# Performance work log

Hardware: AMD Instinct MI355X
Metric: run time of the kernel (lower is better)

The kernel has to match this reference:

```python
import jax, jax.numpy as jnp
import numpy as np

B, T, E = 4, 2048, 1024
H, D = 16, 64  # num_heads, head_size; H*D == E


def setup_inputs() -> dict:
    key = jax.random.key(0)
    ks = jax.random.split(key, 8)
    s = 0.02
    x = jax.random.normal(ks[0], (B, T, E), dtype=jnp.float32)
    attention_mask = jnp.ones((B, T), dtype=jnp.float32)
    # stacked per-head projection weights (no bias), torch Linear: y = x @ W.T
    Wq = jax.random.normal(ks[1], (H, E, D), dtype=jnp.float32) * s
    Wk = jax.random.normal(ks[2], (H, E, D), dtype=jnp.float32) * s
    Wv = jax.random.normal(ks[3], (H, E, D), dtype=jnp.float32) * s
    Wo = jax.random.normal(ks[4], (E, E), dtype=jnp.float32) * s
    bo = jnp.zeros((E,), dtype=jnp.float32)
    return {"x": x, "attention_mask": attention_mask, "Wq": Wq, "Wk": Wk,
            "Wv": Wv, "Wo": Wo, "bo": bo}


def reference(x, attention_mask, Wq, Wk, Wv, Wo, bo):
    # per-head projections, vectorized over heads: [B,T,E] x [H,E,D] -> [B,H,T,D]
    q = jnp.einsum('bte,hed->bhtd', x, Wq)
    k = jnp.einsum('bte,hed->bhtd', x, Wk)
    v = jnp.einsum('bte,hed->bhtd', x, Wv)
    scores = jnp.einsum('bhtd,bhsd->bhts', q, k) / jnp.sqrt(jnp.float32(D))
    # causal mask (tril): masked_fill with -inf
    causal = jnp.tril(jnp.ones((T, T), dtype=bool))
    scores = jnp.where(causal[None, None, :, :], scores, -jnp.inf)
    # padding mask: weights += (1 - mask) * finfo(float32).min, broadcast over queries
    neg = jnp.finfo(jnp.float32).min
    scores = scores + ((1.0 - attention_mask) * neg)[:, None, None, :]
    weights = jax.nn.softmax(scores, axis=-1)
    out = jnp.einsum('bhts,bhsd->bthd', weights, v).reshape(B, T, H * D)
    return out @ Wo.T + bo
```

## Files before the change

### kernel.cpp

```cpp
#include <hip/hip_runtime.h>
#include <hip/hip_bf16.h>

#define B_ 4
#define T_ 2048
#define E_ 1024
#define H_ 16
#define D_ 64
#define M_ (B_*T_)

typedef short bf16x8 __attribute__((ext_vector_type(8)));
typedef float f32x4  __attribute__((ext_vector_type(4)));
typedef float f32x16 __attribute__((ext_vector_type(16)));

__device__ __forceinline__ short f2bf(float f) {
    __hip_bfloat16 h = __float2bfloat16(f);
    return *reinterpret_cast<short*>(&h);
}

__device__ __forceinline__ void async_ld16(const void* g, void* l) {
    __builtin_amdgcn_global_load_lds(
        (const __attribute__((address_space(1))) unsigned int*)g,
        (__attribute__((address_space(3))) unsigned int*)l, 16, 0, 0);
}

__global__ void conv_bf16(const float* __restrict__ src, short* __restrict__ dst) {
    const int i = blockIdx.x * 256 + threadIdx.x;
    float4 v = ((const float4*)src)[i];
    short4 o = make_short4(f2bf(v.x), f2bf(v.y), f2bf(v.z), f2bf(v.w));
    ((short4*)dst)[i] = o;
}

__global__ void bias_prep(const float* __restrict__ mask, float* __restrict__ bias) {
    const int i = blockIdx.x * 256 + threadIdx.x;
    float bm = (1.0f - mask[i]) * -3.402823466e38f;
    bias[i] = fmaf(bm, 1.4426950f, -8.6561700f);
}

__global__ void wtrans(const float* __restrict__ Wq,
                       const float* __restrict__ Wk,
                       const float* __restrict__ Wv,
                       short* __restrict__ Wt) {
    const int which = blockIdx.z;
    const float* __restrict__ W = (which == 0) ? Wq : (which == 1) ? Wk : Wv;
    const int h  = blockIdx.y;
    const int e0 = blockIdx.x * 64;

    __shared__ float tile[64][65];
    const int tid = threadIdx.x;

#pragma unroll
    for (int r = 0; r < 4; ++r) {
        int lin = tid + r * 256;
        int er = lin >> 4, c4 = (lin & 15) * 4;
        float4 v = *(const float4*)(W + ((size_t)h * E_ + e0 + er) * D_ + c4);
        tile[er][c4 + 0] = v.x; tile[er][c4 + 1] = v.y;
        tile[er][c4 + 2] = v.z; tile[er][c4 + 3] = v.w;
    }
    __syncthreads();
#pragma unroll
    for (int r = 0; r < 4; ++r) {
        int lin = tid + r * 256;
        int dr = lin >> 4, j4 = (lin & 15) * 4;
        short4 o = make_short4(f2bf(tile[j4 + 0][dr]), f2bf(tile[j4 + 1][dr]),
                               f2bf(tile[j4 + 2][dr]), f2bf(tile[j4 + 3][dr]));
        *(short4*)(Wt + ((size_t)which * 1024 + h * 64 + dr) * E_ + e0 + j4) = o;
    }
}

template <int MODE>
__global__ __launch_bounds__(256) void mfma_gemm(
        const short* __restrict__ A,
        const short* __restrict__ Bt,
        short* __restrict__ qo, short* __restrict__ ko, short* __restrict__ vo,
        float* __restrict__ Cout, const float* __restrict__ bo) {
    __shared__ __align__(16) short As[128 * 32];
    __shared__ __align__(16) short Bs[128 * 32];

    const int tid  = threadIdx.x;
    const int wave = tid >> 6, lane = tid & 63;
    const int c = lane & 15, quad = lane >> 4;
    const int wm = wave >> 1, wn = wave & 1;
    const int m0 = blockIdx.x * 128;
    const int n0 = blockIdx.y * 128;

    int rowS[2], kgS[2];
#pragma unroll
    for (int r = 0; r < 2; ++r) {
        int p = r * 256 + wave * 64 + lane;
        rowS[r] = p >> 2;
        kgS[r]  = (p & 3) ^ ((rowS[r] >> 1) & 3);
    }

    f32x4 acc[4][4] = {};

    for (int k0 = 0; k0 < 1024; k0 += 32) {
#pragma unroll
        for (int r = 0; r < 2; ++r) {
            async_ld16(A  + (size_t)(m0 + rowS[r]) * 1024 + k0 + kgS[r] * 8,
                       As + (r * 256 + wave * 64) * 8);
            async_ld16(Bt + (size_t)(n0 + rowS[r]) * 1024 + k0 + kgS[r] * 8,
                       Bs + (r * 256 + wave * 64) * 8);
        }
        __syncthreads();

        bf16x8 af[4], bf[4];
#pragma unroll
        for (int mi = 0; mi < 4; ++mi) {
            int row = wm * 64 + mi * 16 + c;
            int pos = row * 4 + (quad ^ ((row >> 1) & 3));
            af[mi] = *(const bf16x8*)(As + pos * 8);
        }
#pragma unroll
        for (int ni = 0; ni < 4; ++ni) {
            int row = wn * 64 + ni * 16 + c;
            int pos = row * 4 + (quad ^ ((row >> 1) & 3));
            bf[ni] = *(const bf16x8*)(Bs + pos * 8);
        }
#pragma unroll
        for (int mi = 0; mi < 4; ++mi)
#pragma unroll
            for (int ni = 0; ni < 4; ++ni)
                acc[mi][ni] = __builtin_amdgcn_mfma_f32_16x16x32_bf16(
                    af[mi], bf[ni], acc[mi][ni], 0, 0, 0);
        __syncthreads();
    }

    if (MODE == 0) {
        const int which = n0 >> 10;
        const int nb = n0 & 1023;
        if (which == 2) {
#pragma unroll
            for (int mi = 0; mi < 4; ++mi) {
                const int m = m0 + wm * 64 + mi * 16 + quad * 4;
                const int b = m >> 11, t = m & 2047;
#pragma unroll
                for (int ni = 0; ni < 4; ++ni) {
                    const int n = nb + wn * 64 + ni * 16 + c;
                    const int h = n >> 6, d = n & 63;
                    short4 s4 = make_short4(f2bf(acc[mi][ni][0]), f2bf(acc[mi][ni][1]),
                                            f2bf(acc[mi][ni][2]), f2bf(acc[mi][ni][3]));
                    *(short4*)(vo + (((size_t)b * H_ + h) * D_ + d) * T_ + t) = s4;
                }
            }
        } else {
            short* __restrict__ outp = (which == 0) ? qo : ko;
            const float sc = (which == 0) ? 0.18033688f : 1.0f;
#pragma unroll
            for (int mi = 0; mi < 4; ++mi) {
#pragma unroll
                for (int i = 0; i < 4; ++i) {
                    const int m = m0 + wm * 64 + mi * 16 + quad * 4 + i;
                    const int b = m >> 11, t = m & 2047;
#pragma unroll
                    for (int ni = 0; ni < 4; ++ni) {
                        const int n = nb + wn * 64 + ni * 16 + c;
                        const int h = n >> 6, d = n & 63;
                        outp[(((size_t)b * H_ + h) * T_ + t) * D_ + d] =
                            f2bf(acc[mi][ni][i] * sc);
                    }
                }
            }
        }
    } else {
#pragma unroll
        for (int mi = 0; mi < 4; ++mi) {
#pragma unroll
            for (int i = 0; i < 4; ++i) {
                const int m = m0 + wm * 64 + mi * 16 + quad * 4 + i;
#pragma unroll
                for (int ni = 0; ni < 4; ++ni) {
                    const int n = n0 + wn * 64 + ni * 16 + c;
                    Cout[(size_t)m * E_ + n] = acc[mi][ni][i] + bo[n];
                }
            }
        }
    }
}

__global__ __launch_bounds__(512, 4) void flash_attn6(
        const short* __restrict__ qg,
        const short* __restrict__ kg,
        const short* __restrict__ vtg,
        const float* __restrict__ biasg,
        short* __restrict__ attn) {
    const int h = blockIdx.x, b = blockIdx.y;
    const int kb = 7 - blockIdx.z;
    const int tid  = threadIdx.x;
    const int wave = tid >> 6, lane = tid & 63;
    const int ln = lane & 31, hi = lane >> 5;
    const int q0w = kb * 256 + wave * 32;
    const int mytile = 8 * kb + wave;
    const int nt = 8 * kb + 8;

    __shared__ __align__(16) char lds[41984];

    const size_t bh = (size_t)b * H_ + h;
    const short* qbh  = qg  + bh * (size_t)T_ * D_;
    const short* kbh  = kg  + bh * (size_t)T_ * D_;
    const short* vtbh = vtg + bh * (size_t)D_ * T_;
    const float* biasb = biasg + (size_t)b * T_;

    const bool stK = (tid < 256);
    const int t2 = tid & 255;
    const int ks = t2 >> 3, kgs = (t2 & 7) ^ (ks & 7);
    const int vd = t2 >> 2, vgs = ((t2 & 3) - (vd >> 1)) & 3;

    int kaddr[4];
#pragma unroll
    for (int kc = 0; kc < 4; ++kc)
        kaddr[kc] = ln * 128 + ((((kc << 1) + hi) ^ (ln & 7)) << 4);
    int vaddr[4];
#pragma unroll
    for (int dh = 0; dh < 2; ++dh)
#pragma unroll
        for (int kc2 = 0; kc2 < 2; ++kc2) {
            int d = dh * 32 + ln;
            vaddr[dh * 2 + kc2] =
                4096 + d * 64 + (((((kc2 << 1) + hi) + (d >> 1)) & 3) << 4);
        }

    bf16x8 qf[4];
#pragma unroll
    for (int kc = 0; kc < 4; ++kc)
        qf[kc] = *(const bf16x8*)(qbh + (size_t)(q0w + ln) * D_ + kc * 16 + hi * 8);

    async_ld16(biasb + ((wave << 6) + lane) * 4, lds + 32768 + wave * 1024);

#define STAGE_T(tt2) do {                                                   \
        const int _s0 = (tt2) << 5;                                         \
        const int _bb = ((tt2) & 3) * 8192;                                 \
        if (stK) async_ld16(kbh + (size_t)(_s0 + ks) * D_ + (kgs << 3),     \
                            lds + _bb + (wave & 3) * 1024);                 \
        else     async_ld16(vtbh + (size_t)vd * T_ + _s0 + (vgs << 3),      \
                            lds + _bb + 4096 + (wave & 3) * 1024);          \
    } while (0)

    STAGE_T(0);
    STAGE_T(1);

    f32x16 O0 = {}, O1 = {};
    float lacc = 0.0f;

    for (int tt = 0; tt < nt; ++tt) {
        if (tt + 2 < nt) STAGE_T(tt + 2);
        const int rem = nt - 1 - tt;
        if (rem >= 2)      asm volatile("s_waitcnt vmcnt(2)" ::: "memory");
        else if (rem == 1) asm volatile("s_waitcnt vmcnt(1)" ::: "memory");
        else               asm volatile("s_waitcnt vmcnt(0)" ::: "memory");
        __builtin_amdgcn_s_barrier();

        if (tt <= mytile) {
            const int s0 = tt << 5;
            const int bb = (tt & 3) * 8192;

            f32x4 b4[4];
#pragma unroll
            for (int g = 0; g < 4; ++g)
                b4[g] = *(const f32x4*)(lds + 32768 + (s0 + g * 8 + hi * 4) * 4);

            f32x16 S = {};
            __builtin_amdgcn_s_setprio(1);
#pragma unroll
            for (int kc = 0; kc < 4; ++kc) {
                bf16x8 ka = *(const bf16x8*)(lds + bb + kaddr[kc]);
                S = __builtin_amdgcn_mfma_f32_32x32x16_bf16(ka, qf[kc], S, 0, 0, 0);
            }
            __builtin_amdgcn_s_setprio(0);

            float p[16];
#pragma unroll
            for (int r = 0; r < 16; ++r) {
                float bb2 = ((const float*)&b4[r >> 2])[r & 3];
                p[r] = __builtin_amdgcn_exp2f(S[r] + bb2);
            }
            if (tt == mytile) {
#pragma unroll
                for (int r = 0; r < 16; ++r)
                    if (((r & 3) + ((r >> 2) << 3) + (hi << 2)) > ln)
                        p[r] = 0.0f;
            }
            {
                float t0 = (p[0] + p[1]) + (p[2] + p[3]);
                float t1 = (p[4] + p[5]) + (p[6] + p[7]);
                float t2s = (p[8] + p[9]) + (p[10] + p[11]);
                float t3 = (p[12] + p[13]) + (p[14] + p[15]);
                lacc += (t0 + t1) + (t2s + t3);
            }

            unsigned int u0, u1, u2, u3, u4, u5, u6, u7;
            asm("v_cvt_pk_bf16_f32 %0, %1, %2" : "=v"(u0) : "v"(p[0]),  "v"(p[1]));
            asm("v_cvt_pk_bf16_f32 %0, %1, %2" : "=v"(u1) : "v"(p[2]),  "v"(p[3]));
            asm("v_cvt_pk_bf16_f32 %0, %1, %2" : "=v"(u2) : "v"(p[4]),  "v"(p[5]));
            asm("v_cvt_pk_bf16_f32 %0, %1, %2" : "=v"(u3) : "v"(p[6]),  "v"(p[7]));
            asm("v_cvt_pk_bf16_f32 %0, %1, %2" : "=v"(u4) : "v"(p[8]),  "v"(p[9]));
            asm("v_cvt_pk_bf16_f32 %0, %1, %2" : "=v"(u5) : "v"(p[10]), "v"(p[11]));
            asm("v_cvt_pk_bf16_f32 %0, %1, %2" : "=v"(u6) : "v"(p[12]), "v"(p[13]));
            asm("v_cvt_pk_bf16_f32 %0, %1, %2" : "=v"(u7) : "v"(p[14]), "v"(p[15]));
            asm("v_permlane32_swap_b32 %0, %1" : "+v"(u0), "+v"(u2));
            asm("v_permlane32_swap_b32 %0, %1" : "+v"(u1), "+v"(u3));
            asm("v_permlane32_swap_b32 %0, %1" : "+v"(u4), "+v"(u6));
            asm("v_permlane32_swap_b32 %0, %1" : "+v"(u5), "+v"(u7));
            union { unsigned int w[4]; bf16x8 v; } pa0, pa1;
            pa0.w[0] = u0; pa0.w[1] = u1; pa0.w[2] = u2; pa0.w[3] = u3;
            pa1.w[0] = u4; pa1.w[1] = u5; pa1.w[2] = u6; pa1.w[3] = u7;

            bf16x8 v00 = *(const bf16x8*)(lds + bb + vaddr[0]);
            bf16x8 v01 = *(const bf16x8*)(lds + bb + vaddr[1]);
            bf16x8 v10 = *(const bf16x8*)(lds + bb + vaddr[2]);
            bf16x8 v11 = *(const bf16x8*)(lds + bb + vaddr[3]);
            __builtin_amdgcn_s_setprio(1);
            O0 = __builtin_amdgcn_mfma_f32_32x32x16_bf16(pa0.v, v00, O0, 0, 0, 0);
            O0 = __builtin_amdgcn_mfma_f32_32x32x16_bf16(pa1.v, v01, O0, 0, 0, 0);
            O1 = __builtin_amdgcn_mfma_f32_32x32x16_bf16(pa0.v, v10, O1, 0, 0, 0);
            O1 = __builtin_amdgcn_mfma_f32_32x32x16_bf16(pa1.v, v11, O1, 0, 0, 0);
            __builtin_amdgcn_s_setprio(0);
        }
    }
#undef STAGE_T

    unsigned int la = __float_as_uint(lacc), lb2 = la;
    asm("v_permlane32_swap_b32 %0, %1" : "+v"(la), "+v"(lb2));
    const float ltot = __uint_as_float(la) + __uint_as_float(lb2);

    float* lsh = (float*)(lds + 40960) + wave * 32;
    if (hi == 0) lsh[ln] = 1.0f / ltot;
    __syncthreads();

    short* ab = attn + (size_t)b * T_ * E_ + h * D_;
#pragma unroll
    for (int r = 0; r < 16; ++r) {
        const int qrow = (r & 3) + ((r >> 2) << 3) + (hi << 2);
        const float iv = lsh[qrow];
        const size_t base = (size_t)(q0w + qrow) * E_;
        ab[base + ln]      = f2bf(O0[r] * iv);
        ab[base + 32 + ln] = f2bf(O1[r] * iv);
    }
}

extern "C" void kernel_launch(void* const* d_in, const int* in_sizes, int n_in,
                              void* d_out, int out_size, void* d_ws, size_t ws_size,
                              hipStream_t stream) {
    const float* x    = (const float*)d_in[0];
    const float* mask = (const float*)d_in[1];
    const float* Wq   = (const float*)d_in[2];
    const float* Wk   = (const float*)d_in[3];
    const float* Wv   = (const float*)d_in[4];
    const float* Wo   = (const float*)d_in[5];
    const float* bo   = (const float*)d_in[6];
    float* out        = (float*)d_out;

    const size_t S = (size_t)M_ * E_;
    char* ws = (char*)d_ws;
    short* xb   = (short*)ws;
    short* qb   = (short*)(ws + S * 2);
    short* kb   = (short*)(ws + S * 4);
    short* vtb  = (short*)(ws + S * 6);
    short* Wt   = (short*)(ws + S * 8);
    short* Wob  = (short*)(ws + S * 8 + (size_t)3 * 1024 * 1024 * 2);
    float* bias = (float*)(ws + S * 8 + (size_t)4 * 1024 * 1024 * 2);
    short* attnb = xb;

    conv_bf16<<<dim3(M_ * E_ / 1024), 256, 0, stream>>>(x, xb);
    conv_bf16<<<dim3(E_ * E_ / 1024), 256, 0, stream>>>(Wo, Wob);
    wtrans<<<dim3(E_ / 64, H_, 3), 256, 0, stream>>>(Wq, Wk, Wv, Wt);
    bias_prep<<<dim3(B_ * T_ / 256), 256, 0, stream>>>(mask, bias);

    mfma_gemm<0><<<dim3(M_ / 128, 3 * E_ / 128), 256, 0, stream>>>(
        xb, Wt, qb, kb, vtb, nullptr, nullptr);

    flash_attn6<<<dim3(H_, B_, 8), 512, 0, stream>>>(qb, kb, vtb, bias, attnb);

    mfma_gemm<1><<<dim3(M_ / 128, E_ / 128), 256, 0, stream>>>(
        attnb, Wob, nullptr, nullptr, nullptr, out, bo);
}
```

Measured before the change: 256.5 us.

## Triple-buffer GEMM LDS tiles with async prefetch two stages ahead

Replaces the single-buffered K loop of the MFMA GEMM with a three-stage LDS ring. Global-to-LDS async loads are issued two tiles ahead, and a partial vmcnt wait plus a single barrier per iteration replaces two __syncthreads. Wave priority is raised around the MFMA block. The aim is to overlap global memory latency with compute, at the cost of tripling the shared memory per block (48KB), which may lower occupancy.

```diff
diff --git a/kernel.cpp b/kernel.cpp
--- a/kernel.cpp
+++ b/kernel.cpp
@@ -73,8 +73,8 @@
         const short* __restrict__ Bt,
         short* __restrict__ qo, short* __restrict__ ko, short* __restrict__ vo,
         float* __restrict__ Cout, const float* __restrict__ bo) {
-    __shared__ __align__(16) short As[128 * 32];
-    __shared__ __align__(16) short Bs[128 * 32];
+    __shared__ __align__(16) short As[3][128 * 32];
+    __shared__ __align__(16) short Bs[3][128 * 32];
 
     const int tid  = threadIdx.x;
     const int wave = tid >> 6, lane = tid & 63;
@@ -93,37 +93,55 @@
 
     f32x4 acc[4][4] = {};
 
-    for (int k0 = 0; k0 < 1024; k0 += 32) {
-#pragma unroll
-        for (int r = 0; r < 2; ++r) {
-            async_ld16(A  + (size_t)(m0 + rowS[r]) * 1024 + k0 + kgS[r] * 8,
-                       As + (r * 256 + wave * 64) * 8);
-            async_ld16(Bt + (size_t)(n0 + rowS[r]) * 1024 + k0 + kgS[r] * 8,
-                       Bs + (r * 256 + wave * 64) * 8);
-        }
-        __syncthreads();
-
+#define STAGE(kt2, bu) do {                                                  \
+        const int _k0 = (kt2) * 32;                                          \
+        _Pragma("unroll")                                                    \
+        for (int r = 0; r < 2; ++r) {                                        \
+            async_ld16(A  + (size_t)(m0 + rowS[r]) * 1024 + _k0 + kgS[r] * 8,\
+                       &As[bu][(r * 256 + wave * 64) * 8]);                  \
+            async_ld16(Bt + (size_t)(n0 + rowS[r]) * 1024 + _k0 + kgS[r] * 8,\
+                       &Bs[bu][(r * 256 + wave * 64) * 8]);                  \
+        }                                                                    \
+    } while (0)
+
+    STAGE(0, 0);
+    STAGE(1, 1);
+
+    int bi = 0, wbuf = 2;
+    for (int kt = 0; kt < 32; ++kt) {
+        if (kt < 31) asm volatile("s_waitcnt vmcnt(4)" ::: "memory");
+        else         asm volatile("s_waitcnt vmcnt(0)" ::: "memory");
+        __builtin_amdgcn_s_barrier();
+        if (kt + 2 < 32) STAGE(kt + 2, wbuf);
+
+        const short* __restrict__ as = As[bi];
+        const short* __restrict__ bs = Bs[bi];
         bf16x8 af[4], bf[4];
 #pragma unroll
         for (int mi = 0; mi < 4; ++mi) {
             int row = wm * 64 + mi * 16 + c;
             int pos = row * 4 + (quad ^ ((row >> 1) & 3));
-            af[mi] = *(const bf16x8*)(As + pos * 8);
+            af[mi] = *(const bf16x8*)(as + pos * 8);
         }
 #pragma unroll
         for (int ni = 0; ni < 4; ++ni) {
             int row = wn * 64 + ni * 16 + c;
             int pos = row * 4 + (quad ^ ((row >> 1) & 3));
-            bf[ni] = *(const bf16x8*)(Bs + pos * 8);
-        }
+            bf[ni] = *(const bf16x8*)(bs + pos * 8);
+        }
+        __builtin_amdgcn_s_setprio(1);
 #pragma unroll
         for (int mi = 0; mi < 4; ++mi)
 #pragma unroll
             for (int ni = 0; ni < 4; ++ni)
                 acc[mi][ni] = __builtin_amdgcn_mfma_f32_16x16x32_bf16(
                     af[mi], bf[ni], acc[mi][ni], 0, 0, 0);
-        __syncthreads();
-    }
+        __builtin_amdgcn_s_setprio(0);
+
+        bi = (bi == 2) ? 0 : bi + 1;
+        wbuf = (wbuf == 2) ? 0 : wbuf + 1;
+    }
+#undef STAGE
 
     if (MODE == 0) {
         const int which = n0 >> 10;
```

Result: no change. 257.1 us (+0.2%).

## Rewrite MFMA GEMM with 256x128 tiles, triple-buffered LDS and ping-pong scheduling

Applied to the files above, without the earlier changes.

The projection and output GEMMs now use 512-thread blocks with 256x128 tiles and a K-step of 64. They stage A and B into a three-deep LDS ring with async global-to-LDS loads and explicit vmcnt waits. Each K-step is split into two MFMA phases separated by barriers and s_setprio, so loads for future stages overlap with compute. The aim is to hide global memory latency and raise MFMA utilization, at the cost of 144KB LDS per block, fragile manual waitcnt accounting, and fewer blocks in the grid.

```diff
diff --git a/kernel.cpp b/kernel.cpp
--- a/kernel.cpp
+++ b/kernel.cpp
@@ -68,62 +68,112 @@
 }
 
 template <int MODE>
-__global__ __launch_bounds__(256) void mfma_gemm(
+__global__ __launch_bounds__(512, 2) void mfma_gemm(
         const short* __restrict__ A,
         const short* __restrict__ Bt,
         short* __restrict__ qo, short* __restrict__ ko, short* __restrict__ vo,
         float* __restrict__ Cout, const float* __restrict__ bo) {
-    __shared__ __align__(16) short As[128 * 32];
-    __shared__ __align__(16) short Bs[128 * 32];
+    __shared__ __align__(16) char lds[3 * 49152];
 
     const int tid  = threadIdx.x;
     const int wave = tid >> 6, lane = tid & 63;
     const int c = lane & 15, quad = lane >> 4;
     const int wm = wave >> 1, wn = wave & 1;
-    const int m0 = blockIdx.x * 128;
+    const int m0 = blockIdx.x * 256;
     const int n0 = blockIdx.y * 128;
 
-    int rowS[2], kgS[2];
-#pragma unroll
-    for (int r = 0; r < 2; ++r) {
-        int p = r * 256 + wave * 64 + lane;
-        rowS[r] = p >> 2;
-        kgS[r]  = (p & 3) ^ ((rowS[r] >> 1) & 3);
+    const int rr = tid >> 3;
+    const int cc = (tid & 7) ^ (rr & 7);
+
+    int aoff[4], boff[4];
+#pragma unroll
+    for (int mi = 0; mi < 4; ++mi) {
+        int row = wm * 64 + mi * 16 + c;
+        aoff[mi] = row * 128 + ((quad ^ (row & 7)) << 4);
+    }
+#pragma unroll
+    for (int ni = 0; ni < 4; ++ni) {
+        int row = wn * 64 + ni * 16 + c;
+        boff[ni] = 32768 + row * 128 + ((quad ^ (row & 7)) << 4);
     }
 
     f32x4 acc[4][4] = {};
 
-    for (int k0 = 0; k0 < 1024; k0 += 32) {
-#pragma unroll
-        for (int r = 0; r < 2; ++r) {
-            async_ld16(A  + (size_t)(m0 + rowS[r]) * 1024 + k0 + kgS[r] * 8,
-                       As + (r * 256 + wave * 64) * 8);
-            async_ld16(Bt + (size_t)(n0 + rowS[r]) * 1024 + k0 + kgS[r] * 8,
-                       Bs + (r * 256 + wave * 64) * 8);
+#define STGU(bufb, k0v, u) do {                                              \
+        const short* _s = ((u) < 4) ? A : Bt;                                \
+        const int _b0 = ((u) < 4) ? (m0 + (u) * 64) : (n0 + ((u) - 4) * 64); \
+        const int _do = ((u) < 4) ? ((u) * 8192) : (32768 + ((u) - 4) * 8192);\
+        async_ld16(_s + (size_t)(_b0 + rr) * 1024 + (k0v) + cc * 8,          \
+                   lds + (bufb) + _do + wave * 1024);                        \
+    } while (0)
+
+#pragma unroll
+    for (int u = 0; u < 6; ++u) STGU(0, 0, u);
+#pragma unroll
+    for (int u = 0; u < 6; ++u) STGU(49152, 64, u);
+    asm volatile("s_waitcnt vmcnt(6)" ::: "memory");
+    __builtin_amdgcn_s_barrier();
+
+    int rbase = 0;
+#pragma unroll 1
+    for (int k = 0; k < 16; ++k) {
+        const char* rb = lds + rbase;
+        const int wbase = (rbase == 0) ? 98304 : rbase - 49152;
+        const int kw = (k + 2) * 64;
+
+        bf16x8 a_[4][2], b01[2][2];
+#pragma unroll
+        for (int mi = 0; mi < 4; ++mi)
+#pragma unroll
+            for (int ks = 0; ks < 2; ++ks)
+                a_[mi][ks] = *(const bf16x8*)(rb + (aoff[mi] ^ (ks << 6)));
+#pragma unroll
+        for (int ni = 0; ni < 2; ++ni)
+#pragma unroll
+            for (int ks = 0; ks < 2; ++ks)
+                b01[ni][ks] = *(const bf16x8*)(rb + (boff[ni] ^ (ks << 6)));
+        if (k < 14) {
+            STGU(wbase, kw, 0); STGU(wbase, kw, 1);
+            STGU(wbase, kw, 2); STGU(wbase, kw, 3);
         }
-        __syncthreads();
-
-        bf16x8 af[4], bf[4];
-#pragma unroll
-        for (int mi = 0; mi < 4; ++mi) {
-            int row = wm * 64 + mi * 16 + c;
-            int pos = row * 4 + (quad ^ ((row >> 1) & 3));
-            af[mi] = *(const bf16x8*)(As + pos * 8);
-        }
-#pragma unroll
-        for (int ni = 0; ni < 4; ++ni) {
-            int row = wn * 64 + ni * 16 + c;
-            int pos = row * 4 + (quad ^ ((row >> 1) & 3));
-            bf[ni] = *(const bf16x8*)(Bs + pos * 8);
-        }
+        __builtin_amdgcn_s_barrier();
+        __builtin_amdgcn_s_setprio(1);
 #pragma unroll
         for (int mi = 0; mi < 4; ++mi)
 #pragma unroll
-            for (int ni = 0; ni < 4; ++ni)
-                acc[mi][ni] = __builtin_amdgcn_mfma_f32_16x16x32_bf16(
-                    af[mi], bf[ni], acc[mi][ni], 0, 0, 0);
-        __syncthreads();
-    }
+            for (int ni = 0; ni < 2; ++ni)
+#pragma unroll
+                for (int ks = 0; ks < 2; ++ks)
+                    acc[mi][ni] = __builtin_amdgcn_mfma_f32_16x16x32_bf16(
+                        a_[mi][ks], b01[ni][ks], acc[mi][ni], 0, 0, 0);
+        __builtin_amdgcn_s_setprio(0);
+        __builtin_amdgcn_s_barrier();
+
+        bf16x8 b23[2][2];
+#pragma unroll
+        for (int ni = 0; ni < 2; ++ni)
+#pragma unroll
+            for (int ks = 0; ks < 2; ++ks)
+                b23[ni][ks] = *(const bf16x8*)(rb + (boff[2 + ni] ^ (ks << 6)));
+        if (k < 14) { STGU(wbase, kw, 4); STGU(wbase, kw, 5); }
+        if (k < 14)       asm volatile("s_waitcnt vmcnt(6)" ::: "memory");
+        else if (k == 14) asm volatile("s_waitcnt vmcnt(0)" ::: "memory");
+        __builtin_amdgcn_s_barrier();
+        __builtin_amdgcn_s_setprio(1);
+#pragma unroll
+        for (int mi = 0; mi < 4; ++mi)
+#pragma unroll
+            for (int ni = 0; ni < 2; ++ni)
+#pragma unroll
+                for (int ks = 0; ks < 2; ++ks)
+                    acc[mi][2 + ni] = __builtin_amdgcn_mfma_f32_16x16x32_bf16(
+                        a_[mi][ks], b23[ni][ks], acc[mi][2 + ni], 0, 0, 0);
+        __builtin_amdgcn_s_setprio(0);
+        __builtin_amdgcn_s_barrier();
+
+        rbase = (rbase == 98304) ? 0 : rbase + 49152;
+    }
+#undef STGU
 
     if (MODE == 0) {
         const int which = n0 >> 10;
@@ -365,11 +415,11 @@
     wtrans<<<dim3(E_ / 64, H_, 3), 256, 0, stream>>>(Wq, Wk, Wv, Wt);
     bias_prep<<<dim3(B_ * T_ / 256), 256, 0, stream>>>(mask, bias);
 
-    mfma_gemm<0><<<dim3(M_ / 128, 3 * E_ / 128), 256, 0, stream>>>(
+    mfma_gemm<0><<<dim3(M_ / 256, 3 * E_ / 128), 512, 0, stream>>>(
         xb, Wt, qb, kb, vtb, nullptr, nullptr);
 
     flash_attn6<<<dim3(H_, B_, 8), 512, 0, stream>>>(qb, kb, vtb, bias, attnb);
 
-    mfma_gemm<1><<<dim3(M_ / 128, E_ / 128), 256, 0, stream>>>(
+    mfma_gemm<1><<<dim3(M_ / 256, E_ / 128), 512, 0, stream>>>(
         attnb, Wob, nullptr, nullptr, nullptr, out, bo);
 }
```

Measured after the change: 252.0 us. About the same (-1.7%).
